# Kernel optimization log

Hardware: AMD Instinct MI355X
Metric: run time of the kernel (lower is better)

The kernel has to match this reference:

```python
import jax, jax.numpy as jnp
import numpy as np

S, B, D, H = 2048, 2, 1024, 16
DK = D // H  # 64

def setup_inputs() -> dict:
    key = jax.random.key(0)
    ks = jax.random.split(key, 11)
    scale = 1.0 / np.sqrt(D)
    return {
        "query": jax.random.normal(ks[0], (S, B, D), dtype=jnp.float32),
        "key":   jax.random.normal(ks[1], (S, B, D), dtype=jnp.float32),
        "value": jax.random.normal(ks[2], (S, B, D), dtype=jnp.float32),
        "Wq": jax.random.normal(ks[3], (D, D), dtype=jnp.float32) * scale,
        "bq": jax.random.normal(ks[4], (D,), dtype=jnp.float32) * scale,
        "Wk": jax.random.normal(ks[5], (D, D), dtype=jnp.float32) * scale,
        "bk": jax.random.normal(ks[6], (D,), dtype=jnp.float32) * scale,
        "Wv": jax.random.normal(ks[7], (D, D), dtype=jnp.float32) * scale,
        "bv": jax.random.normal(ks[8], (D,), dtype=jnp.float32) * scale,
        "Wo": jax.random.normal(ks[9], (D, D), dtype=jnp.float32) * scale,
        "bo": jax.random.normal(ks[10], (D,), dtype=jnp.float32) * scale,
    }

def _split_heads(x):
    # [S, B, D] -> [H, B, S, DK]  (matches .view(S,B,H,DK).transpose(0,2))
    return x.reshape(S, B, H, DK).transpose(2, 1, 0, 3)

def reference(query, key, value, Wq, bq, Wk, bk, Wv, bv, Wo, bo):
    q = _split_heads(query @ Wq.T + bq)
    k = _split_heads(key   @ Wk.T + bk)
    v = _split_heads(value @ Wv.T + bv)
    scores = jnp.einsum('hbqd,hbkd->hbqk', q, k) / jnp.sqrt(jnp.float32(DK))
    align = jax.nn.softmax(scores, axis=-1)
    x = jnp.einsum('hbqk,hbkd->hbqd', align, v)  # [H,B,S,DK]
    x = x.transpose(2, 1, 0, 3).reshape(S, B, D)  # back to [S,B,D]
    return x @ Wo.T + bo
```

## Files before the change

kernel.cpp:

```cpp
#include <hip/hip_runtime.h>
#include <math.h>

#define SS 2048
#define BB 2
#define DD 1024
#define HH 16
#define DKK 64
#define MM (SS*BB)

typedef _Float16 f16;
typedef __attribute__((ext_vector_type(8))) _Float16 f16x8;
typedef __attribute__((ext_vector_type(4))) float f32x4;

__device__ __forceinline__ void gload_lds16(const void* g, void* l) {
    __builtin_amdgcn_global_load_lds(
        (const __attribute__((address_space(1))) unsigned*)g,
        (__attribute__((address_space(3))) unsigned*)l, 16, 0, 0);
}

__global__ __launch_bounds__(256)
void cvt_x(const float* __restrict__ q, const float* __restrict__ k,
           const float* __restrict__ v, f16* __restrict__ out)
{
    const int z = blockIdx.y;
    const float* src = z == 0 ? q : (z == 1 ? k : v);
    size_t t = (size_t)blockIdx.x*256 + threadIdx.x;
    float4 f0 = ((const float4*)src)[t*2];
    float4 f1 = ((const float4*)src)[t*2+1];
    union { f16 h[8]; uint4 u; } r;
    r.h[0]=(f16)f0.x; r.h[1]=(f16)f0.y; r.h[2]=(f16)f0.z; r.h[3]=(f16)f0.w;
    r.h[4]=(f16)f1.x; r.h[5]=(f16)f1.y; r.h[6]=(f16)f1.z; r.h[7]=(f16)f1.w;
    ((uint4*)(out + (size_t)z*MM*DD))[t] = r.u;
}

__global__ __launch_bounds__(256)
void cvt_w(const float* __restrict__ wq, const float* __restrict__ wk,
           const float* __restrict__ wv, const float* __restrict__ wo,
           f16* __restrict__ out)
{
    const int z = blockIdx.y;
    const float* src = z == 0 ? wq : (z == 1 ? wk : (z == 2 ? wv : wo));
    size_t t = (size_t)blockIdx.x*256 + threadIdx.x;
    float4 f0 = ((const float4*)src)[t*2];
    float4 f1 = ((const float4*)src)[t*2+1];
    union { f16 h[8]; uint4 u; } r;
    r.h[0]=(f16)f0.x; r.h[1]=(f16)f0.y; r.h[2]=(f16)f0.z; r.h[3]=(f16)f0.w;
    r.h[4]=(f16)f1.x; r.h[5]=(f16)f1.y; r.h[6]=(f16)f1.z; r.h[7]=(f16)f1.w;
    ((uint4*)(out + (size_t)z*DD*DD))[t] = r.u;
}

__global__ __launch_bounds__(256)
void qkv_gemm(const f16* __restrict__ A16, const f16* __restrict__ W16,
              const float* __restrict__ bq, const float* __restrict__ bk,
              const float* __restrict__ bv,
              f16* __restrict__ Qh, f16* __restrict__ Kh, f16* __restrict__ Vt)
{
    __shared__ __align__(16) f16 As[128*32];
    __shared__ __align__(16) f16 Bs[128*32];

    const int tid  = threadIdx.x;
    const int w    = tid >> 6;
    const int lane = tid & 63;
    const int ln   = lane & 15;
    const int quad = lane >> 4;
    const int z  = blockIdx.z;
    const int m0 = blockIdx.x * 128;
    const int n0 = blockIdx.y * 128;
    const int wm = (w >> 1) * 64;
    const int wn = (w & 1) * 64;

    const f16* A = A16 + (size_t)z*MM*DD;
    const f16* W = W16 + (size_t)z*DD*DD;
    const float* bias = z == 0 ? bq : (z == 1 ? bk : bv);

    f32x4 acc[4][4];
    #pragma unroll
    for (int mt = 0; mt < 4; mt++)
        #pragma unroll
        for (int nt = 0; nt < 4; nt++)
            acc[mt][nt] = (f32x4){0.f,0.f,0.f,0.f};

    int slot[2], r_[2], gch[2];
    #pragma unroll
    for (int i = 0; i < 2; i++) {
        slot[i] = i*256 + tid;
        r_[i]   = slot[i] >> 2;
        gch[i]  = ((slot[i] & 3) ^ ((r_[i] >> 1) & 3)) * 8;
    }

    for (int step = 0; step < DD/32; step++) {
        const int k0 = step*32;
        __syncthreads();
        #pragma unroll
        for (int i = 0; i < 2; i++) {
            gload_lds16(A + (size_t)(m0 + r_[i])*DD + k0 + gch[i],
                        (char*)As + slot[i]*16);
            gload_lds16(W + (size_t)(n0 + r_[i])*DD + k0 + gch[i],
                        (char*)Bs + slot[i]*16);
        }
        __syncthreads();

        f16x8 af[4], bf[4];
        #pragma unroll
        for (int mt = 0; mt < 4; mt++) {
            int r = wm + mt*16 + ln;
            af[mt] = *(const f16x8*)&As[r*32 + ((quad ^ ((r>>1)&3)) << 3)];
        }
        #pragma unroll
        for (int nt = 0; nt < 4; nt++) {
            int r = wn + nt*16 + ln;
            bf[nt] = *(const f16x8*)&Bs[r*32 + ((quad ^ ((r>>1)&3)) << 3)];
        }
        #pragma unroll
        for (int mt = 0; mt < 4; mt++)
            #pragma unroll
            for (int nt = 0; nt < 4; nt++)
                acc[mt][nt] = __builtin_amdgcn_mfma_f32_16x16x32_f16(
                    af[mt], bf[nt], acc[mt][nt], 0, 0, 0);
    }

    float bvv[4];
    #pragma unroll
    for (int nt = 0; nt < 4; nt++) bvv[nt] = bias[n0 + wn + nt*16 + ln];

    if (z == 2) {
        #pragma unroll
        for (int mt = 0; mt < 4; mt++) {
            int mbase = m0 + wm + mt*16 + quad*4;
            int s0 = mbase >> 1;
            #pragma unroll
            for (int nt = 0; nt < 4; nt++) {
                int n = n0 + wn + nt*16 + ln;
                int h = n >> 6, d = n & 63;
                float v0 = acc[mt][nt][0] + bvv[nt];
                float v1 = acc[mt][nt][1] + bvv[nt];
                float v2 = acc[mt][nt][2] + bvv[nt];
                float v3 = acc[mt][nt][3] + bvv[nt];
                union { f16 h[2]; unsigned u; } p0, p1;
                p0.h[0] = (f16)v0; p0.h[1] = (f16)v2;
                p1.h[0] = (f16)v1; p1.h[1] = (f16)v3;
                *(unsigned*)&Vt[((size_t)(0*HH + h)*DKK + d)*SS + s0] = p0.u;
                *(unsigned*)&Vt[((size_t)(1*HH + h)*DKK + d)*SS + s0] = p1.u;
            }
        }
    } else {
        const float scale = z == 0 ? 0.125f : 1.0f;
        f16* dst = z == 0 ? Qh : Kh;
        #pragma unroll
        for (int mt = 0; mt < 4; mt++)
            #pragma unroll
            for (int nt = 0; nt < 4; nt++)
                #pragma unroll
                for (int r = 0; r < 4; r++) {
                    int m = m0 + wm + mt*16 + quad*4 + r;
                    int n = n0 + wn + nt*16 + ln;
                    int s = m >> 1, b = m & 1;
                    int h = n >> 6, d = n & 63;
                    dst[(((size_t)(b*HH + h))*SS + s)*DKK + d] =
                        (f16)((acc[mt][nt][r] + bvv[nt]) * scale);
                }
    }
}

__global__ __launch_bounds__(256)
void out_gemm(const f16* __restrict__ A, const f16* __restrict__ W,
              const float* __restrict__ bias, float* __restrict__ out)
{
    __shared__ __align__(16) f16 As[64*32];
    __shared__ __align__(16) f16 Bs[128*32];

    const int tid  = threadIdx.x;
    const int w    = tid >> 6;
    const int lane = tid & 63;
    const int ln   = lane & 15;
    const int quad = lane >> 4;
    const int m0 = blockIdx.x * 64;
    const int n0 = blockIdx.y * 128;
    const int wm = (w >> 1) * 32;
    const int wn = (w & 1) * 64;

    f32x4 acc[2][4];
    #pragma unroll
    for (int mt = 0; mt < 2; mt++)
        #pragma unroll
        for (int nt = 0; nt < 4; nt++)
            acc[mt][nt] = (f32x4){0.f,0.f,0.f,0.f};

    const int rA  = tid >> 2;
    const int gchA = ((tid & 3) ^ ((rA >> 1) & 3)) * 8;
    int slotB[2], rB[2], gchB[2];
    #pragma unroll
    for (int i = 0; i < 2; i++) {
        slotB[i] = i*256 + tid;
        rB[i]    = slotB[i] >> 2;
        gchB[i]  = ((slotB[i] & 3) ^ ((rB[i] >> 1) & 3)) * 8;
    }

    for (int step = 0; step < DD/32; step++) {
        const int k0 = step*32;
        __syncthreads();
        gload_lds16(A + (size_t)(m0 + rA)*DD + k0 + gchA, (char*)As + tid*16);
        #pragma unroll
        for (int i = 0; i < 2; i++)
            gload_lds16(W + (size_t)(n0 + rB[i])*DD + k0 + gchB[i],
                        (char*)Bs + slotB[i]*16);
        __syncthreads();

        f16x8 af[2], bf[4];
        #pragma unroll
        for (int mt = 0; mt < 2; mt++) {
            int r = wm + mt*16 + ln;
            af[mt] = *(const f16x8*)&As[r*32 + ((quad ^ ((r>>1)&3)) << 3)];
        }
        #pragma unroll
        for (int nt = 0; nt < 4; nt++) {
            int r = wn + nt*16 + ln;
            bf[nt] = *(const f16x8*)&Bs[r*32 + ((quad ^ ((r>>1)&3)) << 3)];
        }
        #pragma unroll
        for (int mt = 0; mt < 2; mt++)
            #pragma unroll
            for (int nt = 0; nt < 4; nt++)
                acc[mt][nt] = __builtin_amdgcn_mfma_f32_16x16x32_f16(
                    af[mt], bf[nt], acc[mt][nt], 0, 0, 0);
    }

    #pragma unroll
    for (int nt = 0; nt < 4; nt++) {
        float bvv = bias[n0 + wn + nt*16 + ln];
        #pragma unroll
        for (int mt = 0; mt < 2; mt++)
            #pragma unroll
            for (int r = 0; r < 4; r++) {
                int m = m0 + wm + mt*16 + quad*4 + r;
                int n = n0 + wn + nt*16 + ln;
                out[(size_t)m*DD + n] = acc[mt][nt][r] + bvv;
            }
    }
}

__global__ __launch_bounds__(256)
void attn_v4(const f16* __restrict__ Q, const f16* __restrict__ K,
             const f16* __restrict__ V, f16* __restrict__ Xh)
{
    __shared__ __align__(16) f16 Ks[64*64];
    __shared__ __align__(16) f16 Vs[64*64];
    __shared__ __align__(16) f16 Ps[64*72];

    const int tid  = threadIdx.x;
    const int w    = tid >> 6;
    const int lane = tid & 63;
    const int ln   = lane & 15;
    const int quad = lane >> 4;
    const int h = blockIdx.y, b = blockIdx.z;
    const size_t base  = ((size_t)(b*HH + h)) * SS * DKK;
    const int Q0 = blockIdx.x * 64;

    f16x8 qf[2];
    #pragma unroll
    for (int ks = 0; ks < 2; ks++)
        qf[ks] = *(const f16x8*)(Q + base + (size_t)(Q0 + w*16 + ln)*DKK + ks*32 + quad*8);

    f16x8 ones;
    #pragma unroll
    for (int i = 0; i < 8; i++) ones[i] = (f16)1.0f;

    f32x4 o[4];
    #pragma unroll
    for (int nt = 0; nt < 4; nt++) o[nt] = (f32x4){0.f,0.f,0.f,0.f};
    f32x4 lacc = (f32x4){0.f,0.f,0.f,0.f};

    const int slot0 = tid, slot1 = 256 + tid;
    const int sr0 = slot0 >> 3, sc0 = slot0 & 7;
    const int sr1 = slot1 >> 3, sc1 = slot1 & 7;

    for (int kt = 0; kt < SS/64; kt++) {
        __syncthreads();
        gload_lds16(K + base + (size_t)(kt*64 + sr0)*DKK + ((sc0 ^ (sr0&7)) << 3),
                    (char*)Ks + slot0*16);
        gload_lds16(K + base + (size_t)(kt*64 + sr1)*DKK + ((sc1 ^ (sr1&7)) << 3),
                    (char*)Ks + slot1*16);
        gload_lds16(V + base + (size_t)sr0*SS + kt*64 + ((sc0 ^ (sr0&7)) << 3),
                    (char*)Vs + slot0*16);
        gload_lds16(V + base + (size_t)sr1*SS + kt*64 + ((sc1 ^ (sr1&7)) << 3),
                    (char*)Vs + slot1*16);
        __syncthreads();

        f32x4 sc[4];
        #pragma unroll
        for (int nt = 0; nt < 4; nt++) sc[nt] = (f32x4){0.f,0.f,0.f,0.f};
        #pragma unroll
        for (int ks = 0; ks < 2; ks++) {
            #pragma unroll
            for (int nt = 0; nt < 4; nt++) {
                int key = nt*16 + ln;
                f16x8 kb = *(const f16x8*)&Ks[key*64 + (((ks*4+quad) ^ (key&7)) << 3)];
                sc[nt] = __builtin_amdgcn_mfma_f32_16x16x32_f16(qf[ks], kb, sc[nt], 0, 0, 0);
            }
        }

        #pragma unroll
        for (int nt = 0; nt < 4; nt++)
            #pragma unroll
            for (int r = 0; r < 4; r++)
                Ps[(w*16 + quad*4 + r)*72 + nt*16 + ln] = (f16)__expf(sc[nt][r]);

        #pragma unroll
        for (int ks = 0; ks < 2; ks++) {
            f16x8 pa = *(const f16x8*)&Ps[(w*16 + ln)*72 + ks*32 + quad*8];
            lacc = __builtin_amdgcn_mfma_f32_16x16x32_f16(pa, ones, lacc, 0, 0, 0);
            #pragma unroll
            for (int nt = 0; nt < 4; nt++) {
                int d = nt*16 + ln;
                f16x8 vb = *(const f16x8*)&Vs[d*64 + (((ks*4+quad) ^ (d&7)) << 3)];
                o[nt] = __builtin_amdgcn_mfma_f32_16x16x32_f16(pa, vb, o[nt], 0, 0, 0);
            }
        }
    }

    #pragma unroll
    for (int r = 0; r < 4; r++) {
        float inv = 1.0f / lacc[r];
        int s = Q0 + w*16 + quad*4 + r;
        f16* xp = Xh + ((size_t)s*BB + b)*DD + h*DKK + ln;
        #pragma unroll
        for (int nt = 0; nt < 4; nt++)
            xp[nt*16] = (f16)(o[nt][r] * inv);
    }
}

extern "C" void kernel_launch(void* const* d_in, const int* in_sizes, int n_in,
                              void* d_out, int out_size, void* d_ws, size_t ws_size,
                              hipStream_t stream) {
    (void)in_sizes; (void)n_in; (void)out_size; (void)ws_size;
    const float* query = (const float*)d_in[0];
    const float* key   = (const float*)d_in[1];
    const float* value = (const float*)d_in[2];
    const float* Wq = (const float*)d_in[3];
    const float* bq = (const float*)d_in[4];
    const float* Wk = (const float*)d_in[5];
    const float* bk = (const float*)d_in[6];
    const float* Wv = (const float*)d_in[7];
    const float* bv = (const float*)d_in[8];
    const float* Wo = (const float*)d_in[9];
    const float* bo = (const float*)d_in[10];

    char* ws = (char*)d_ws;
    f16* A16 = (f16*)ws;
    f16* W16 = (f16*)(ws + 25165824);
    f16* Qh  = (f16*)(ws + 33554432);
    f16* Kh  = (f16*)(ws + 41943040);
    f16* Vt  = (f16*)(ws + 50331648);
    f16* Xh  = (f16*)(ws + 58720256);

    cvt_x<<<dim3(MM*DD/8/256, 3), 256, 0, stream>>>(query, key, value, A16);
    cvt_w<<<dim3(DD*DD/8/256, 4), 256, 0, stream>>>(Wq, Wk, Wv, Wo, W16);

    qkv_gemm<<<dim3(MM/128, DD/128, 3), 256, 0, stream>>>(
        A16, W16, bq, bk, bv, Qh, Kh, Vt);

    attn_v4<<<dim3(SS/64, HH, BB), 256, 0, stream>>>(Qh, Kh, Vt, Xh);

    out_gemm<<<dim3(MM/64, DD/128), 256, 0, stream>>>(
        Xh, W16 + (size_t)3*DD*DD, bo, (float*)d_out);
}
```

Measured before the change: 236.0 us.

## Rewrite attention with 32x32x16 MFMA, 128-query tiles, transposed score layout

```diff
diff --git a/kernel.cpp b/kernel.cpp
--- a/kernel.cpp
+++ b/kernel.cpp
@@ -10,8 +10,15 @@
 
 typedef _Float16 f16;
 typedef __attribute__((ext_vector_type(8))) _Float16 f16x8;
+typedef __attribute__((ext_vector_type(2))) __fp16 fp16x2r;
 typedef __attribute__((ext_vector_type(4))) float f32x4;
-
+typedef __attribute__((ext_vector_type(16))) float f32x16;
+
+__device__ __forceinline__ unsigned pk2(float a, float b) {
+    union { fp16x2r h; unsigned u; } v;
+    v.h = __builtin_amdgcn_cvt_pkrtz(a, b);
+    return v.u;
+}
 __device__ __forceinline__ void gload_lds16(const void* g, void* l) {
     __builtin_amdgcn_global_load_lds(
         (const __attribute__((address_space(1))) unsigned*)g,
@@ -27,10 +34,10 @@
     size_t t = (size_t)blockIdx.x*256 + threadIdx.x;
     float4 f0 = ((const float4*)src)[t*2];
     float4 f1 = ((const float4*)src)[t*2+1];
-    union { f16 h[8]; uint4 u; } r;
-    r.h[0]=(f16)f0.x; r.h[1]=(f16)f0.y; r.h[2]=(f16)f0.z; r.h[3]=(f16)f0.w;
-    r.h[4]=(f16)f1.x; r.h[5]=(f16)f1.y; r.h[6]=(f16)f1.z; r.h[7]=(f16)f1.w;
-    ((uint4*)(out + (size_t)z*MM*DD))[t] = r.u;
+    uint4 r;
+    r.x = pk2(f0.x, f0.y); r.y = pk2(f0.z, f0.w);
+    r.z = pk2(f1.x, f1.y); r.w = pk2(f1.z, f1.w);
+    ((uint4*)(out + (size_t)z*MM*DD))[t] = r;
 }
 
 __global__ __launch_bounds__(256)
@@ -43,10 +50,10 @@
     size_t t = (size_t)blockIdx.x*256 + threadIdx.x;
     float4 f0 = ((const float4*)src)[t*2];
     float4 f1 = ((const float4*)src)[t*2+1];
-    union { f16 h[8]; uint4 u; } r;
-    r.h[0]=(f16)f0.x; r.h[1]=(f16)f0.y; r.h[2]=(f16)f0.z; r.h[3]=(f16)f0.w;
-    r.h[4]=(f16)f1.x; r.h[5]=(f16)f1.y; r.h[6]=(f16)f1.z; r.h[7]=(f16)f1.w;
-    ((uint4*)(out + (size_t)z*DD*DD))[t] = r.u;
+    uint4 r;
+    r.x = pk2(f0.x, f0.y); r.y = pk2(f0.z, f0.w);
+    r.z = pk2(f1.x, f1.y); r.w = pk2(f1.z, f1.w);
+    ((uint4*)(out + (size_t)z*DD*DD))[t] = r;
 }
 
 __global__ __launch_bounds__(256)
@@ -136,11 +143,8 @@
                 float v1 = acc[mt][nt][1] + bvv[nt];
                 float v2 = acc[mt][nt][2] + bvv[nt];
                 float v3 = acc[mt][nt][3] + bvv[nt];
-                union { f16 h[2]; unsigned u; } p0, p1;
-                p0.h[0] = (f16)v0; p0.h[1] = (f16)v2;
-                p1.h[0] = (f16)v1; p1.h[1] = (f16)v3;
-                *(unsigned*)&Vt[((size_t)(0*HH + h)*DKK + d)*SS + s0] = p0.u;
-                *(unsigned*)&Vt[((size_t)(1*HH + h)*DKK + d)*SS + s0] = p1.u;
+                *(unsigned*)&Vt[((size_t)(0*HH + h)*DKK + d)*SS + s0] = pk2(v0, v2);
+                *(unsigned*)&Vt[((size_t)(1*HH + h)*DKK + d)*SS + s0] = pk2(v1, v3);
             }
         }
     } else {
@@ -240,39 +244,39 @@
 }
 
 __global__ __launch_bounds__(256)
-void attn_v4(const f16* __restrict__ Q, const f16* __restrict__ K,
+void attn_v5(const f16* __restrict__ Q, const f16* __restrict__ K,
              const f16* __restrict__ V, f16* __restrict__ Xh)
 {
     __shared__ __align__(16) f16 Ks[64*64];
     __shared__ __align__(16) f16 Vs[64*64];
-    __shared__ __align__(16) f16 Ps[64*72];
+    __shared__ __align__(16) f16 Pl[4*32*72];
 
     const int tid  = threadIdx.x;
     const int w    = tid >> 6;
     const int lane = tid & 63;
-    const int ln   = lane & 15;
-    const int quad = lane >> 4;
+    const int l5   = lane & 31;
+    const int hf   = lane >> 5;
     const int h = blockIdx.y, b = blockIdx.z;
-    const size_t base  = ((size_t)(b*HH + h)) * SS * DKK;
-    const int Q0 = blockIdx.x * 64;
-
-    f16x8 qf[2];
-    #pragma unroll
-    for (int ks = 0; ks < 2; ks++)
-        qf[ks] = *(const f16x8*)(Q + base + (size_t)(Q0 + w*16 + ln)*DKK + ks*32 + quad*8);
+    const size_t base = ((size_t)(b*HH + h)) * SS * DKK;
+    const int Q0 = blockIdx.x * 128;
+
+    f16x8 qf[4];
+    #pragma unroll
+    for (int ks = 0; ks < 4; ks++)
+        qf[ks] = *(const f16x8*)(Q + base + (size_t)(Q0 + w*32 + l5)*DKK + ks*16 + hf*8);
 
     f16x8 ones;
     #pragma unroll
     for (int i = 0; i < 8; i++) ones[i] = (f16)1.0f;
 
-    f32x4 o[4];
-    #pragma unroll
-    for (int nt = 0; nt < 4; nt++) o[nt] = (f32x4){0.f,0.f,0.f,0.f};
-    f32x4 lacc = (f32x4){0.f,0.f,0.f,0.f};
+    f32x16 o[2];
+    o[0] = (f32x16)(0.f); o[1] = (f32x16)(0.f);
+    f32x16 lacc = (f32x16)(0.f);
 
     const int slot0 = tid, slot1 = 256 + tid;
     const int sr0 = slot0 >> 3, sc0 = slot0 & 7;
     const int sr1 = slot1 >> 3, sc1 = slot1 & 7;
+    f16* const myP = &Pl[w*2304 + l5*72];
 
     for (int kt = 0; kt < SS/64; kt++) {
         __syncthreads();
@@ -286,47 +290,59 @@
                     (char*)Vs + slot1*16);
         __syncthreads();
 
-        f32x4 sc[4];
-        #pragma unroll
-        for (int nt = 0; nt < 4; nt++) sc[nt] = (f32x4){0.f,0.f,0.f,0.f};
-        #pragma unroll
-        for (int ks = 0; ks < 2; ks++) {
-            #pragma unroll
-            for (int nt = 0; nt < 4; nt++) {
-                int key = nt*16 + ln;
-                f16x8 kb = *(const f16x8*)&Ks[key*64 + (((ks*4+quad) ^ (key&7)) << 3)];
-                sc[nt] = __builtin_amdgcn_mfma_f32_16x16x32_f16(qf[ks], kb, sc[nt], 0, 0, 0);
-            }
-        }
-
-        #pragma unroll
-        for (int nt = 0; nt < 4; nt++)
-            #pragma unroll
-            for (int r = 0; r < 4; r++)
-                Ps[(w*16 + quad*4 + r)*72 + nt*16 + ln] = (f16)__expf(sc[nt][r]);
-
-        #pragma unroll
-        for (int ks = 0; ks < 2; ks++) {
-            f16x8 pa = *(const f16x8*)&Ps[(w*16 + ln)*72 + ks*32 + quad*8];
-            lacc = __builtin_amdgcn_mfma_f32_16x16x32_f16(pa, ones, lacc, 0, 0, 0);
-            #pragma unroll
-            for (int nt = 0; nt < 4; nt++) {
-                int d = nt*16 + ln;
-                f16x8 vb = *(const f16x8*)&Vs[d*64 + (((ks*4+quad) ^ (d&7)) << 3)];
-                o[nt] = __builtin_amdgcn_mfma_f32_16x16x32_f16(pa, vb, o[nt], 0, 0, 0);
-            }
-        }
-    }
-
-    #pragma unroll
-    for (int r = 0; r < 4; r++) {
-        float inv = 1.0f / lacc[r];
-        int s = Q0 + w*16 + quad*4 + r;
-        f16* xp = Xh + ((size_t)s*BB + b)*DD + h*DKK + ln;
-        #pragma unroll
-        for (int nt = 0; nt < 4; nt++)
-            xp[nt*16] = (f16)(o[nt][r] * inv);
-    }
+        f32x16 sc[2];
+        sc[0] = (f32x16)(0.f); sc[1] = (f32x16)(0.f);
+        #pragma unroll
+        for (int ks = 0; ks < 4; ks++) {
+            const int cc = ks*2 + hf;
+            #pragma unroll
+            for (int mt = 0; mt < 2; mt++) {
+                int key = mt*32 + l5;
+                f16x8 ka = *(const f16x8*)&Ks[key*64 + ((cc ^ (key&7)) << 3)];
+                sc[mt] = __builtin_amdgcn_mfma_f32_32x32x16_f16(ka, qf[ks], sc[mt], 0, 0, 0);
+            }
+        }
+
+        #pragma unroll
+        for (int mt = 0; mt < 2; mt++)
+            #pragma unroll
+            for (int g = 0; g < 4; g++) {
+                float p0 = __expf(sc[mt][g*4+0]);
+                float p1 = __expf(sc[mt][g*4+1]);
+                float p2 = __expf(sc[mt][g*4+2]);
+                float p3 = __expf(sc[mt][g*4+3]);
+                uint2 pk;
+                pk.x = pk2(p0, p1);
+                pk.y = pk2(p2, p3);
+                *(uint2*)&myP[mt*32 + g*8 + hf*4] = pk;
+            }
+
+        #pragma unroll
+        for (int ks = 0; ks < 4; ks++) {
+            f16x8 pb = *(const f16x8*)&myP[ks*16 + hf*8];
+            lacc = __builtin_amdgcn_mfma_f32_32x32x16_f16(ones, pb, lacc, 0, 0, 0);
+            const int cc = ks*2 + hf;
+            #pragma unroll
+            for (int mt = 0; mt < 2; mt++) {
+                int d = mt*32 + l5;
+                f16x8 va = *(const f16x8*)&Vs[d*64 + ((cc ^ (d&7)) << 3)];
+                o[mt] = __builtin_amdgcn_mfma_f32_32x32x16_f16(va, pb, o[mt], 0, 0, 0);
+            }
+        }
+    }
+
+    const float inv = 1.0f / lacc[0];
+    const int qg = Q0 + w*32 + l5;
+    f16* xp = Xh + ((size_t)qg*BB + b)*DD + h*DKK;
+    #pragma unroll
+    for (int mt = 0; mt < 2; mt++)
+        #pragma unroll
+        for (int g = 0; g < 4; g++) {
+            uint2 pk;
+            pk.x = pk2(o[mt][g*4+0]*inv, o[mt][g*4+1]*inv);
+            pk.y = pk2(o[mt][g*4+2]*inv, o[mt][g*4+3]*inv);
+            *(uint2*)&xp[mt*32 + g*8 + hf*4] = pk;
+        }
 }
 
 extern "C" void kernel_launch(void* const* d_in, const int* in_sizes, int n_in,
@@ -359,7 +375,7 @@
     qkv_gemm<<<dim3(MM/128, DD/128, 3), 256, 0, stream>>>(
         A16, W16, bq, bk, bv, Qh, Kh, Vt);
 
-    attn_v4<<<dim3(SS/64, HH, BB), 256, 0, stream>>>(Qh, Kh, Vt, Xh);
+    attn_v5<<<dim3(SS/128, HH, BB), 256, 0, stream>>>(Qh, Kh, Vt, Xh);
 
     out_gemm<<<dim3(MM/64, DD/128), 256, 0, stream>>>(
         Xh, W16 + (size_t)3*DD*DD, bo, (float*)d_out);
```

Result: faster. 229.8 us (-2.6%).
